# Kernel tuning notes

Hardware: AMD Instinct MI355X
Metric: run time of the kernel (lower is better)

## Reference

```python
import jax, jax.numpy as jnp
import numpy as np

B, R, L = 1024, 10, 512  # batch, num_rounds, lstm_size
EPS = 1e-10


def _gated(x, Wy, by, Wg, bg):
    # GatedTrans: tanh(Linear(x)) * sigmoid(Linear(x)); dropout is identity in eval
    return jnp.tanh(x @ Wy + by) * jax.nn.sigmoid(x @ Wg + bg)


def setup_inputs() -> dict:
    key = jax.random.key(0)
    ks = jax.random.split(key, 16)
    s_in = 1.0 / np.sqrt(2 * L)
    s_hid = 1.0 / np.sqrt(L)
    inp = {
        "hist": jax.random.normal(ks[0], (B, R, 2 * L), jnp.float32),
        "ques": jax.random.normal(ks[1], (B, R, 2 * L), jnp.float32),
        "noise": jax.random.uniform(ks[2], (B, R, R), jnp.float32),
        # H_embed GatedTrans params
        "Wy_h": jax.random.normal(ks[3], (2 * L, L), jnp.float32) * s_in,
        "by_h": jnp.zeros((L,), jnp.float32),
        "Wg_h": jax.random.normal(ks[4], (2 * L, L), jnp.float32) * s_in,
        "bg_h": jnp.zeros((L,), jnp.float32),
        # Q_embed GatedTrans params
        "Wy_q": jax.random.normal(ks[5], (2 * L, L), jnp.float32) * s_in,
        "by_q": jnp.zeros((L,), jnp.float32),
        "Wg_q": jax.random.normal(ks[6], (2 * L, L), jnp.float32) * s_in,
        "bg_q": jnp.zeros((L,), jnp.float32),
        # MLP: Linear(2L->L), Linear(L->1)
        "W1": jax.random.normal(ks[7], (2 * L, L), jnp.float32) * s_in,
        "b1": jnp.zeros((L,), jnp.float32),
        "W2": jax.random.normal(ks[8], (L, 1), jnp.float32) * s_hid,
        "b2": jnp.zeros((1,), jnp.float32),
        # att: Linear(2->1)
        "Wa": jax.random.normal(ks[9], (2, 1), jnp.float32) * 0.7,
        "ba": jnp.zeros((1,), jnp.float32),
    }
    return inp


def _forward(hist, ques, noise, Wy_h, by_h, Wg_h, bg_h, Wy_q, by_q, Wg_q, bg_q,
             W1, b1, W2, b2, Wa, ba):
    h = _gated(hist, Wy_h, by_h, Wg_h, bg_h)  # [B,R,L], indexed by j (history round)
    q = _gated(ques, Wy_q, by_q, Wg_q, bg_q)  # [B,R,L], indexed by i (question round)
    # MLP layer 1 on concat(h_j, q_i) without materializing the 2L concat:
    sh = h @ W1[:L] + b1            # [B,R,L] (j part + bias)
    sq = q @ W1[L:]                 # [B,R,L] (i part)
    hid = sq[:, :, None, :] + sh[:, None, :, :]  # [B,R(i),R(j),L]
    score = (hid @ W2 + b2)[..., 0]              # [B,R,R]
    # delta_t = cumsum over rows of lower-triangular ones
    tri = jnp.tril(jnp.ones((R, R), jnp.float32))
    delta_t = jnp.cumsum(tri, axis=0)            # [R,R]
    # att Linear(2->1) on concat(score, delta_t)
    logits = score * Wa[0, 0] + delta_t * Wa[1, 0] + ba[0]  # [B,R,R]
    # per-round Gumbel softmax over prefix [:i+1], vectorized with tril mask
    g = -jnp.log(EPS - jnp.log(noise + EPS))     # Gumbel(0,1) noise
    mask = tri.astype(bool)                       # [R,R], True for j<=i
    z = jnp.where(mask, logits + g, -1e9)
    y_soft = jax.nn.softmax(z, axis=-1)           # temperature = 1
    one_hot = jax.nn.one_hot(jnp.argmax(z, axis=-1), R, dtype=logits.dtype)
    # straight-through: value = one_hot, gradient flows through y_soft (valid cols only)
    y = one_hot + (y_soft - jax.lax.stop_gradient(y_soft)) * tri
    return y


def reference(hist, ques, noise, Wy_h, by_h, Wg_h, bg_h, Wy_q, by_q, Wg_q, bg_q,
              W1, b1, W2, b2, Wa, ba):
    return _forward(hist, ques, noise, Wy_h, by_h, Wg_h, bg_h, Wy_q, by_q,
                    Wg_q, bg_q, W1, b1, W2, b2, Wa, ba)
```

## Files before the change

### kernel.cpp

```cpp
#include <hip/hip_runtime.h>
#include <math.h>

typedef float f4 __attribute__((ext_vector_type(4)));
typedef float f32x4 __attribute__((ext_vector_type(4)));
typedef _Float16 h4 __attribute__((ext_vector_type(4)));
typedef _Float16 h8 __attribute__((ext_vector_type(8)));

#define NB 1024
#define NR 10
#define NL 512
#define NM (NB*NR)
#define NK (2*NL)

#define BIMG_OFF   131072ull
#define BIMG_EMBED 4194304ull
#define AIMG_OFF   (BIMG_OFF + 2ull*BIMG_EMBED)
#define AIMG_EMBED (80ull*32ull*16384ull)
#define WS_NEED2   (AIMG_OFF + 2ull*AIMG_EMBED)

#define SCALE_A 16.0f
#define SCALE_B 512.0f
#define INV_SCALE (1.0f/8192.0f)

__device__ __forceinline__ void gl_lds16(const void* g, void* s) {
    __builtin_amdgcn_global_load_lds(
        (const __attribute__((address_space(1))) unsigned int*)g,
        (__attribute__((address_space(3))) unsigned int*)s, 16, 0, 0);
}

__global__ __launch_bounds__(256) void k_prep(
    const float* __restrict__ hist, const float* __restrict__ ques,
    const float* __restrict__ Wy_h, const float* __restrict__ Wg_h,
    const float* __restrict__ Wy_q, const float* __restrict__ Wg_q,
    const float* __restrict__ W1, const float* __restrict__ b1,
    const float* __restrict__ W2, const float* __restrict__ b2,
    char* __restrict__ Aimg, char* __restrict__ Bimg,
    float* __restrict__ vh, float* __restrict__ vq, float* __restrict__ cc,
    float* __restrict__ tzero)
{
    __shared__ float Ws[32][68];
    __shared__ float red[4];
    const int bid = blockIdx.x;
    const int t = threadIdx.x;

    if (bid < 5120) {
        const int rb = bid % 80, ks = (bid / 80) % 32, z = bid / 2560;
        const float* X = z ? ques : hist;
        char* dst = Aimg + (size_t)z*AIMG_EMBED + ((size_t)(rb*32 + ks))*16384;
        #pragma unroll
        for (int i = 0; i < 2; ++i) {
            const int m   = i*4 + (t >> 6);
            const int row = m*16 + (t & 15);
            const int kg  = (t >> 4) & 3;
            const float* src = X + (size_t)(rb*128 + row)*NK + ks*32 + kg*8;
            f4 a0 = *(const f4*)src;
            f4 a1 = *(const f4*)(src + 4);
            h8 hi, lo;
            #pragma unroll
            for (int j = 0; j < 4; ++j) {
                float x0 = a0[j] * SCALE_A;
                _Float16 h0 = (_Float16)x0;
                hi[j] = h0; lo[j] = (_Float16)(x0 - (float)h0);
                float x1 = a1[j] * SCALE_A;
                _Float16 h1 = (_Float16)x1;
                hi[4+j] = h1; lo[4+j] = (_Float16)(x1 - (float)h1);
            }
            *(h8*)(dst + i*4096 + t*16) = hi;
            *(h8*)(dst + 8192 + i*4096 + t*16) = lo;
        }
    } else if (bid < 6144) {
        const int wb = bid - 5120;
        const int nh = wb % 8, ks = (wb / 8) % 32, mi = wb / 256;
        const float* W = (mi==0) ? Wy_h : (mi==1) ? Wg_h : (mi==2) ? Wy_q : Wg_q;
        const int emb = mi >> 1, nfb = (mi & 1) * 4;
        const int kl = t >> 4, nl4 = (t & 15) * 4;
        #pragma unroll
        for (int i = 0; i < 2; ++i) {
            f4 wv = *(const f4*)(W + (size_t)(ks*32 + kl + 16*i)*NL + nh*64 + nl4);
            *(f4*)&Ws[kl + 16*i][nl4] = wv;
        }
        __syncthreads();
        const int kg = t >> 6, nl = t & 63;
        h8 hi, lo;
        #pragma unroll
        for (int e8 = 0; e8 < 8; ++e8) {
            float x = Ws[kg*8 + e8][nl] * SCALE_B;
            _Float16 h = (_Float16)x;
            hi[e8] = h;
            lo[e8] = (_Float16)(x - (float)h);
        }
        const int nf  = nfb + (nl >> 4);
        const int l16 = (nl & 15) + 16*kg;
        char* p = Bimg + (size_t)emb*BIMG_EMBED
                + ((size_t)(nh*32 + ks)*2)*8192 + nf*1024 + l16*16;
        *(h8*)p = hi;
        *(h8*)(p + 8192) = lo;
    } else if (bid < 7169) {
        const int o = bid - 6144;
        const float* row = (o < 1024) ? (W1 + (size_t)o*NL) : b1;
        float s = fmaf(row[t], W2[t], row[t+256]*W2[t+256]);
        #pragma unroll
        for (int d = 1; d < 64; d <<= 1) s += __shfl_xor(s, d);
        if ((t & 63) == 0) red[t >> 6] = s;
        __syncthreads();
        if (t == 0) {
            float tot = red[0] + red[1] + red[2] + red[3];
            if (o < 512) vh[o] = tot;
            else if (o < 1024) vq[o-512] = tot;
            else cc[0] = tot + b2[0];
        }
    } else {
        const int zb = bid - 7169;
        f4 zz = {0.f, 0.f, 0.f, 0.f};
        *(f4*)(tzero + (size_t)zb*1024 + t*4) = zz;
    }
}

__global__ __launch_bounds__(256, 2) void k_embed_mfma3(
    const char* __restrict__ Aimg, const char* __restrict__ Bimg,
    const float* __restrict__ by_h, const float* __restrict__ bg_h,
    const float* __restrict__ by_q, const float* __restrict__ bg_q,
    const float* __restrict__ vv, float* __restrict__ tout)
{
    const int z = blockIdx.z, nt = blockIdx.y, rb = blockIdx.x;
    const float* by = z ? by_q : by_h;
    const float* bg = z ? bg_q : bg_h;
    const float* v  = vv + z*NL;
    float* tptr = tout + (size_t)z*NM;
    const char* At = Aimg + (size_t)z*AIMG_EMBED + ((size_t)rb*32)*16384;
    const char* Bt = Bimg + (size_t)z*BIMG_EMBED + (size_t)nt*32*16384;

    __shared__ char smem[65536];

    const int t = threadIdx.x;
    const int l = t & 63, w = t >> 6;
    const int wr = w >> 1, wc = w & 1;

    f32x4 acc[4][4];
    #pragma unroll
    for (int m = 0; m < 4; ++m)
      #pragma unroll
      for (int n = 0; n < 4; ++n) { f32x4 zz = {0.f,0.f,0.f,0.f}; acc[m][n] = zz; }

    auto stage = [&](int b, int ksrc) {
        const char* ga = At + (size_t)ksrc*16384 + w*4096 + l*16;
        const char* gb = Bt + (size_t)ksrc*16384 + w*4096 + l*16;
        char* da = smem + b*32768 + w*4096;
        char* db = smem + b*32768 + 16384 + w*4096;
        #pragma unroll
        for (int j = 0; j < 4; ++j) {
            gl_lds16(ga + j*1024, da + j*1024);
            gl_lds16(gb + j*1024, db + j*1024);
        }
    };

    stage(0, 0);
    stage(1, 1);
    asm volatile("s_waitcnt vmcnt(8)" ::: "memory");
    __builtin_amdgcn_s_barrier();

    #pragma unroll 2
    for (int ks = 0; ks < 32; ++ks) {
        const int cur = ks & 1;
        const char* sA = smem + cur*32768;
        const char* sB = sA + 16384;

        h8 av[4][2], bv[4][2];
        #pragma unroll
        for (int m = 0; m < 4; ++m)
          #pragma unroll
          for (int s = 0; s < 2; ++s)
            av[m][s] = *(const h8*)(sA + s*8192 + (wr*4 + m)*1024 + l*16);
        #pragma unroll
        for (int fn = 0; fn < 4; ++fn) {
            const int nf = (fn < 2) ? (wc*2 + fn) : (4 + wc*2 + (fn - 2));
            #pragma unroll
            for (int s = 0; s < 2; ++s)
                bv[fn][s] = *(const h8*)(sB + s*8192 + nf*1024 + l*16);
        }
        asm volatile("s_waitcnt lgkmcnt(0)" ::: "memory");
        __builtin_amdgcn_sched_barrier(0);
        __builtin_amdgcn_s_barrier();
        if (ks + 2 < 32) stage(cur, ks + 2);

        __builtin_amdgcn_s_setprio(1);
        #pragma unroll
        for (int m = 0; m < 4; ++m)
          #pragma unroll
          for (int fn = 0; fn < 4; ++fn) {
            acc[m][fn] = __builtin_amdgcn_mfma_f32_16x16x32_f16(av[m][0], bv[fn][0], acc[m][fn], 0, 0, 0);
            acc[m][fn] = __builtin_amdgcn_mfma_f32_16x16x32_f16(av[m][0], bv[fn][1], acc[m][fn], 0, 0, 0);
            acc[m][fn] = __builtin_amdgcn_mfma_f32_16x16x32_f16(av[m][1], bv[fn][0], acc[m][fn], 0, 0, 0);
          }
        __builtin_amdgcn_s_setprio(0);

        if (ks < 30)       asm volatile("s_waitcnt vmcnt(8)" ::: "memory");
        else if (ks == 30) asm volatile("s_waitcnt vmcnt(0)" ::: "memory");
        if (ks < 31) __builtin_amdgcn_s_barrier();
    }

    const int coll = l & 15, rg = l >> 4;
    #pragma unroll
    for (int m = 0; m < 4; ++m) {
      #pragma unroll
      for (int r = 0; r < 4; ++r) {
        float ps = 0.0f;
        #pragma unroll
        for (int n = 0; n < 2; ++n) {
            const int c = nt*64 + wc*32 + n*16 + coll;
            float y = acc[m][n  ][r]*INV_SCALE + by[c];
            float g = acc[m][n+2][r]*INV_SCALE + bg[c];
            ps += v[c] * (tanhf(y) * (1.0f/(1.0f + expf(-g))));
        }
        ps += __shfl_xor(ps, 1);
        ps += __shfl_xor(ps, 2);
        ps += __shfl_xor(ps, 4);
        ps += __shfl_xor(ps, 8);
        if (coll == 0)
            atomicAdd(&tptr[rb*128 + wr*64 + m*16 + rg*4 + r], ps);
      }
    }
}

__global__ __launch_bounds__(256) void k_vcalc2(const float* __restrict__ W1,
    const float* __restrict__ b1, const float* __restrict__ W2,
    const float* __restrict__ b2, float* __restrict__ vh,
    float* __restrict__ vq, float* __restrict__ cc)
{
    const int o = blockIdx.x;
    const float* row = (o < 1024) ? (W1 + (size_t)o*NL) : b1;
    const int t = threadIdx.x;
    float s = fmaf(row[t], W2[t], row[t+256]*W2[t+256]);
    #pragma unroll
    for (int d = 1; d < 64; d <<= 1) s += __shfl_xor(s, d);
    __shared__ float red[4];
    if ((t & 63) == 0) red[t >> 6] = s;
    __syncthreads();
    if (t == 0) {
        float tot = red[0] + red[1] + red[2] + red[3];
        if (o < 512) vh[o] = tot;
        else if (o < 1024) vq[o-512] = tot;
        else cc[0] = tot + b2[0];
    }
}

__global__ __launch_bounds__(256) void k_embed(const float* __restrict__ X,
    const float* __restrict__ Wy, const float* __restrict__ by,
    const float* __restrict__ Wg, const float* __restrict__ bg,
    const float* __restrict__ v, float* __restrict__ tout)
{
    __shared__ float As[32][68];
    __shared__ float Bys[32][64];
    __shared__ float Bgs[32][64];
    const int tid  = threadIdx.x;
    const int row0 = blockIdx.x * 64;
    const int c0   = blockIdx.y * 64;
    const int tx = tid & 15, ty = tid >> 4;
    float accy[4][4] = {};
    float accg[4][4] = {};
    const int arow = tid >> 3;
    const int ak   = (tid & 7) << 2;
    const int bk   = tid >> 4;
    const int bc   = (tid & 15) << 2;
    const float* Xp0 = X + (size_t)(row0 + arow)*NK + ak;
    const float* Xp1 = Xp0 + (size_t)32*NK;
    for (int k0 = 0; k0 < NK; k0 += 32) {
        f4 a0 = *(const f4*)(Xp0 + k0);
        f4 a1 = *(const f4*)(Xp1 + k0);
        f4 y0 = *(const f4*)&Wy[(size_t)(k0+bk   )*NL + c0 + bc];
        f4 y1 = *(const f4*)&Wy[(size_t)(k0+bk+16)*NL + c0 + bc];
        f4 g0 = *(const f4*)&Wg[(size_t)(k0+bk   )*NL + c0 + bc];
        f4 g1 = *(const f4*)&Wg[(size_t)(k0+bk+16)*NL + c0 + bc];
        #pragma unroll
        for (int j = 0; j < 4; ++j) {
            As[ak+j][arow]      = a0[j];
            As[ak+j][arow + 32] = a1[j];
        }
        *(f4*)&Bys[bk   ][bc] = y0;
        *(f4*)&Bys[bk+16][bc] = y1;
        *(f4*)&Bgs[bk   ][bc] = g0;
        *(f4*)&Bgs[bk+16][bc] = g1;
        __syncthreads();
        #pragma unroll
        for (int kk = 0; kk < 32; ++kk) {
            f4 a   = *(const f4*)&As [kk][ty<<2];
            f4 byv = *(const f4*)&Bys[kk][tx<<2];
            f4 bgv = *(const f4*)&Bgs[kk][tx<<2];
            #pragma unroll
            for (int rr = 0; rr < 4; ++rr)
                #pragma unroll
                for (int cc2 = 0; cc2 < 4; ++cc2) {
                    accy[rr][cc2] = fmaf(a[rr], byv[cc2], accy[rr][cc2]);
                    accg[rr][cc2] = fmaf(a[rr], bgv[cc2], accg[rr][cc2]);
                }
        }
        __syncthreads();
    }
    float rowsum[4] = {0.f, 0.f, 0.f, 0.f};
    #pragma unroll
    for (int rr = 0; rr < 4; ++rr)
        #pragma unroll
        for (int cc2 = 0; cc2 < 4; ++cc2) {
            int c = c0 + (tx<<2) + cc2;
            float xy = accy[rr][cc2] + by[c];
            float xg = accg[rr][cc2] + bg[c];
            float hv = tanhf(xy) * (1.0f / (1.0f + expf(-xg)));
            rowsum[rr] += v[c] * hv;
        }
    float* red = &As[0][0];
    #pragma unroll
    for (int rr = 0; rr < 4; ++rr) red[(ty*4 + rr)*16 + tx] = rowsum[rr];
    __syncthreads();
    if (tid < 64) {
        float s = 0.0f;
        #pragma unroll
        for (int t2 = 0; t2 < 16; ++t2) s += red[tid*16 + t2];
        atomicAdd(&tout[row0 + tid], s);
    }
}

__global__ __launch_bounds__(256) void k_final(const float* __restrict__ th,
    const float* __restrict__ tq, const float* __restrict__ cc,
    const float* __restrict__ noise, const float* __restrict__ Wa,
    const float* __restrict__ ba, float* __restrict__ out)
{
    int idx = blockIdx.x*256 + threadIdx.x;
    if (idx >= NM) return;
    int b = idx / NR, i = idx % NR;
    float wa0 = Wa[0], wa1 = Wa[1], bav = ba[0], c = cc[0];
    float ti = tq[idx];
    const float EPS = 1e-10f;
    float best = -3.0e38f; int am = 0;
    for (int j = 0; j < NR; ++j) {
        float zz;
        if (j <= i) {
            float n = noise[idx*NR + j];
            float g = -logf(EPS - logf(n + EPS));
            float score = ti + th[b*NR + j] + c;
            zz = score*wa0 + (float)(i - j + 1)*wa1 + bav + g;
        } else {
            zz = -1.0e9f;
        }
        if (zz > best) { best = zz; am = j; }
    }
    #pragma unroll
    for (int j = 0; j < NR; ++j) out[idx*NR + j] = (j == am) ? 1.0f : 0.0f;
}

extern "C" void kernel_launch(void* const* d_in, const int* in_sizes, int n_in,
                              void* d_out, int out_size, void* d_ws, size_t ws_size,
                              hipStream_t stream) {
    (void)in_sizes; (void)n_in; (void)out_size;
    const float* hist  = (const float*)d_in[0];
    const float* ques  = (const float*)d_in[1];
    const float* noise = (const float*)d_in[2];
    const float* Wy_h  = (const float*)d_in[3];
    const float* by_h  = (const float*)d_in[4];
    const float* Wg_h  = (const float*)d_in[5];
    const float* bg_h  = (const float*)d_in[6];
    const float* Wy_q  = (const float*)d_in[7];
    const float* by_q  = (const float*)d_in[8];
    const float* Wg_q  = (const float*)d_in[9];
    const float* bg_q  = (const float*)d_in[10];
    const float* W1    = (const float*)d_in[11];
    const float* b1    = (const float*)d_in[12];
    const float* W2    = (const float*)d_in[13];
    const float* b2    = (const float*)d_in[14];
    const float* Wa    = (const float*)d_in[15];
    const float* ba    = (const float*)d_in[16];
    float* out = (float*)d_out;

    float* ws     = (float*)d_ws;
    float* t_h    = ws;
    float* t_q    = ws + NM;
    float* v_h    = ws + 2*NM;
    float* v_q    = v_h + NL;
    float* cconst = v_q + NL;

    if (ws_size >= WS_NEED2) {
        char* Bimg = (char*)d_ws + BIMG_OFF;
        char* Aimg = (char*)d_ws + AIMG_OFF;
        k_prep<<<7189, 256, 0, stream>>>(hist, ques, Wy_h, Wg_h, Wy_q, Wg_q,
            W1, b1, W2, b2, Aimg, Bimg, v_h, v_q, cconst, t_h);
        k_embed_mfma3<<<dim3(80, 8, 2), 256, 0, stream>>>(Aimg, Bimg,
            by_h, bg_h, by_q, bg_q, v_h, t_h);
    } else {
        hipMemsetAsync(t_h, 0, 2*NM*sizeof(float), stream);
        k_vcalc2<<<1025, 256, 0, stream>>>(W1, b1, W2, b2, v_h, v_q, cconst);
        dim3 g(NM/64, NL/64);
        k_embed<<<g, 256, 0, stream>>>(hist, Wy_h, by_h, Wg_h, bg_h, v_h, t_h);
        k_embed<<<g, 256, 0, stream>>>(ques, Wy_q, by_q, Wg_q, bg_q, v_q, t_q);
    }
    k_final<<<(NM + 255)/256, 256, 0, stream>>>(t_h, t_q, cconst, noise, Wa, ba, out);
}
```

Before: 277.7 us.

## Fuse activation fp16 hi/lo split into the MFMA GEMM mainloop

The separate prep pass that converted hist/ques to split-fp16 images in workspace is removed. The GEMM kernel now loads fp32 activations into registers two steps ahead, splits them into hi/lo halves, and writes them into the next LDS buffer itself, while B is still staged with direct global-to-LDS loads. This drops a full write and reread of the activation image (about 80 MB) and shrinks the prep kernel. In exchange the mainloop carries extra VALU conversion work and register pressure, and each activation tile is read and converted again by all 8 N-tile blocks.

```diff
diff --git a/kernel.cpp b/kernel.cpp
--- a/kernel.cpp
+++ b/kernel.cpp
@@ -14,9 +14,7 @@
 
 #define BIMG_OFF   131072ull
 #define BIMG_EMBED 4194304ull
-#define AIMG_OFF   (BIMG_OFF + 2ull*BIMG_EMBED)
-#define AIMG_EMBED (80ull*32ull*16384ull)
-#define WS_NEED2   (AIMG_OFF + 2ull*AIMG_EMBED)
+#define WS_NEED    (BIMG_OFF + 2ull*BIMG_EMBED)
 
 #define SCALE_A 16.0f
 #define SCALE_B 512.0f
@@ -29,12 +27,11 @@
 }
 
 __global__ __launch_bounds__(256) void k_prep(
-    const float* __restrict__ hist, const float* __restrict__ ques,
     const float* __restrict__ Wy_h, const float* __restrict__ Wg_h,
     const float* __restrict__ Wy_q, const float* __restrict__ Wg_q,
     const float* __restrict__ W1, const float* __restrict__ b1,
     const float* __restrict__ W2, const float* __restrict__ b2,
-    char* __restrict__ Aimg, char* __restrict__ Bimg,
+    char* __restrict__ Bimg,
     float* __restrict__ vh, float* __restrict__ vq, float* __restrict__ cc,
     float* __restrict__ tzero)
 {
@@ -43,34 +40,8 @@
     const int bid = blockIdx.x;
     const int t = threadIdx.x;
 
-    if (bid < 5120) {
-        const int rb = bid % 80, ks = (bid / 80) % 32, z = bid / 2560;
-        const float* X = z ? ques : hist;
-        char* dst = Aimg + (size_t)z*AIMG_EMBED + ((size_t)(rb*32 + ks))*16384;
-        #pragma unroll
-        for (int i = 0; i < 2; ++i) {
-            const int m   = i*4 + (t >> 6);
-            const int row = m*16 + (t & 15);
-            const int kg  = (t >> 4) & 3;
-            const float* src = X + (size_t)(rb*128 + row)*NK + ks*32 + kg*8;
-            f4 a0 = *(const f4*)src;
-            f4 a1 = *(const f4*)(src + 4);
-            h8 hi, lo;
-            #pragma unroll
-            for (int j = 0; j < 4; ++j) {
-                float x0 = a0[j] * SCALE_A;
-                _Float16 h0 = (_Float16)x0;
-                hi[j] = h0; lo[j] = (_Float16)(x0 - (float)h0);
-                float x1 = a1[j] * SCALE_A;
-                _Float16 h1 = (_Float16)x1;
-                hi[4+j] = h1; lo[4+j] = (_Float16)(x1 - (float)h1);
-            }
-            *(h8*)(dst + i*4096 + t*16) = hi;
-            *(h8*)(dst + 8192 + i*4096 + t*16) = lo;
-        }
-    } else if (bid < 6144) {
-        const int wb = bid - 5120;
-        const int nh = wb % 8, ks = (wb / 8) % 32, mi = wb / 256;
+    if (bid < 1024) {
+        const int nh = bid % 8, ks = (bid / 8) % 32, mi = bid / 256;
         const float* W = (mi==0) ? Wy_h : (mi==1) ? Wg_h : (mi==2) ? Wy_q : Wg_q;
         const int emb = mi >> 1, nfb = (mi & 1) * 4;
         const int kl = t >> 4, nl4 = (t & 15) * 4;
@@ -95,8 +66,8 @@
                 + ((size_t)(nh*32 + ks)*2)*8192 + nf*1024 + l16*16;
         *(h8*)p = hi;
         *(h8*)(p + 8192) = lo;
-    } else if (bid < 7169) {
-        const int o = bid - 6144;
+    } else if (bid < 2049) {
+        const int o = bid - 1024;
         const float* row = (o < 1024) ? (W1 + (size_t)o*NL) : b1;
         float s = fmaf(row[t], W2[t], row[t+256]*W2[t+256]);
         #pragma unroll
@@ -110,24 +81,25 @@
             else cc[0] = tot + b2[0];
         }
     } else {
-        const int zb = bid - 7169;
+        const int zb = bid - 2049;
         f4 zz = {0.f, 0.f, 0.f, 0.f};
         *(f4*)(tzero + (size_t)zb*1024 + t*4) = zz;
     }
 }
 
-__global__ __launch_bounds__(256, 2) void k_embed_mfma3(
-    const char* __restrict__ Aimg, const char* __restrict__ Bimg,
+__global__ __launch_bounds__(256, 2) void k_embed_mfma4(
+    const float* __restrict__ hist, const float* __restrict__ ques,
+    const char* __restrict__ Bimg,
     const float* __restrict__ by_h, const float* __restrict__ bg_h,
     const float* __restrict__ by_q, const float* __restrict__ bg_q,
     const float* __restrict__ vv, float* __restrict__ tout)
 {
     const int z = blockIdx.z, nt = blockIdx.y, rb = blockIdx.x;
+    const float* X  = z ? ques : hist;
     const float* by = z ? by_q : by_h;
     const float* bg = z ? bg_q : bg_h;
     const float* v  = vv + z*NL;
     float* tptr = tout + (size_t)z*NM;
-    const char* At = Aimg + (size_t)z*AIMG_EMBED + ((size_t)rb*32)*16384;
     const char* Bt = Bimg + (size_t)z*BIMG_EMBED + (size_t)nt*32*16384;
 
     __shared__ char smem[65536];
@@ -136,34 +108,64 @@
     const int l = t & 63, w = t >> 6;
     const int wr = w >> 1, wc = w & 1;
 
+    const int am0 = t >> 6;
+    const float* src1 = X + (size_t)(rb*128 + am0*16 + (t & 15))*NK + ((t >> 4) & 3)*8;
+    const float* src2 = src1 + (size_t)64*NK;
+    const int aw1 = am0*1024 + (t & 63)*16;
+    const int aw2 = aw1 + 4096;
+
+    f4 ar0, ar1, ar2, ar3;
+    auto loadA = [&](int ksrc) {
+        const float* p1 = src1 + ksrc*32;
+        const float* p2 = src2 + ksrc*32;
+        ar0 = *(const f4*)p1; ar1 = *(const f4*)(p1 + 4);
+        ar2 = *(const f4*)p2; ar3 = *(const f4*)(p2 + 4);
+    };
+    auto splitA = [&](char* base) {
+        h8 hi1, lo1, hi2, lo2;
+        #pragma unroll
+        for (int j = 0; j < 4; ++j) {
+            float x0 = ar0[j]*SCALE_A; _Float16 h0 = (_Float16)x0;
+            hi1[j] = h0;   lo1[j] = (_Float16)(x0 - (float)h0);
+            float x1 = ar1[j]*SCALE_A; _Float16 h1 = (_Float16)x1;
+            hi1[4+j] = h1; lo1[4+j] = (_Float16)(x1 - (float)h1);
+            float x2 = ar2[j]*SCALE_A; _Float16 h2 = (_Float16)x2;
+            hi2[j] = h2;   lo2[j] = (_Float16)(x2 - (float)h2);
+            float x3 = ar3[j]*SCALE_A; _Float16 h3 = (_Float16)x3;
+            hi2[4+j] = h3; lo2[4+j] = (_Float16)(x3 - (float)h3);
+        }
+        *(h8*)(base + aw1) = hi1;  *(h8*)(base + 8192 + aw1) = lo1;
+        *(h8*)(base + aw2) = hi2;  *(h8*)(base + 8192 + aw2) = lo2;
+    };
+    auto stageB = [&](int buf, int ksrc) {
+        const char* gb = Bt + (size_t)ksrc*16384 + w*4096 + l*16;
+        char* db = smem + buf*32768 + 16384 + w*4096;
+        #pragma unroll
+        for (int j = 0; j < 4; ++j) gl_lds16(gb + j*1024, db + j*1024);
+    };
+
     f32x4 acc[4][4];
     #pragma unroll
     for (int m = 0; m < 4; ++m)
       #pragma unroll
       for (int n = 0; n < 4; ++n) { f32x4 zz = {0.f,0.f,0.f,0.f}; acc[m][n] = zz; }
 
-    auto stage = [&](int b, int ksrc) {
-        const char* ga = At + (size_t)ksrc*16384 + w*4096 + l*16;
-        const char* gb = Bt + (size_t)ksrc*16384 + w*4096 + l*16;
-        char* da = smem + b*32768 + w*4096;
-        char* db = smem + b*32768 + 16384 + w*4096;
-        #pragma unroll
-        for (int j = 0; j < 4; ++j) {
-            gl_lds16(ga + j*1024, da + j*1024);
-            gl_lds16(gb + j*1024, db + j*1024);
-        }
-    };
-
-    stage(0, 0);
-    stage(1, 1);
-    asm volatile("s_waitcnt vmcnt(8)" ::: "memory");
+    loadA(0);
+    splitA(smem);
+    loadA(1);
+    stageB(0, 0);
+    stageB(1, 1);
+    asm volatile("s_waitcnt lgkmcnt(0)" ::: "memory");
+    asm volatile("s_waitcnt vmcnt(4)" ::: "memory");
     __builtin_amdgcn_s_barrier();
 
     #pragma unroll 2
     for (int ks = 0; ks < 32; ++ks) {
-        const int cur = ks & 1;
+        const int cur = ks & 1, nxt = cur ^ 1;
         const char* sA = smem + cur*32768;
         const char* sB = sA + 16384;
+
+        if (ks < 31) splitA(smem + nxt*32768);
 
         h8 av[4][2], bv[4][2];
         #pragma unroll
@@ -178,10 +180,14 @@
             for (int s = 0; s < 2; ++s)
                 bv[fn][s] = *(const h8*)(sB + s*8192 + nf*1024 + l*16);
         }
+
+        if (ks < 30) loadA(ks + 2);
+
         asm volatile("s_waitcnt lgkmcnt(0)" ::: "memory");
         __builtin_amdgcn_sched_barrier(0);
         __builtin_amdgcn_s_barrier();
-        if (ks + 2 < 32) stage(cur, ks + 2);
+
+        if (ks < 30) stageB(cur, ks + 2);
 
         __builtin_amdgcn_s_setprio(1);
         #pragma unroll
@@ -377,12 +383,11 @@
     float* v_q    = v_h + NL;
     float* cconst = v_q + NL;
 
-    if (ws_size >= WS_NEED2) {
+    if (ws_size >= WS_NEED) {
         char* Bimg = (char*)d_ws + BIMG_OFF;
-        char* Aimg = (char*)d_ws + AIMG_OFF;
-        k_prep<<<7189, 256, 0, stream>>>(hist, ques, Wy_h, Wg_h, Wy_q, Wg_q,
-            W1, b1, W2, b2, Aimg, Bimg, v_h, v_q, cconst, t_h);
-        k_embed_mfma3<<<dim3(80, 8, 2), 256, 0, stream>>>(Aimg, Bimg,
+        k_prep<<<2069, 256, 0, stream>>>(Wy_h, Wg_h, Wy_q, Wg_q,
+            W1, b1, W2, b2, Bimg, v_h, v_q, cconst, t_h);
+        k_embed_mfma4<<<dim3(80, 8, 2), 256, 0, stream>>>(hist, ques, Bimg,
             by_h, bg_h, by_q, bg_q, v_h, t_h);
     } else {
         hipMemsetAsync(t_h, 0, 2*NM*sizeof(float), stream);
```

New measurement: 306.8 us. 1.1x slower.

## Halve embed GEMM N-tile and use triple-buffered LDS pipeline

Applied to the files above, without the earlier changes.

The embed MFMA kernel now computes 32 output columns per block instead of 64, doubling the grid to 80x16x2, and each block loads only its half of the B tile. LDS staging moves from double to triple buffering, so the next-next stage is issued before the current LDS reads and one barrier per iteration is removed. The aim is more blocks for load balance across CUs and better overlap of global loads with MFMA work. In exchange, A tiles are re-read twice as often and each block does less MFMA work per load, and twice as many atomics hit the output.

```diff
diff --git a/kernel.cpp b/kernel.cpp
--- a/kernel.cpp
+++ b/kernel.cpp
@@ -3,7 +3,6 @@
 
 typedef float f4 __attribute__((ext_vector_type(4)));
 typedef float f32x4 __attribute__((ext_vector_type(4)));
-typedef _Float16 h4 __attribute__((ext_vector_type(4)));
 typedef _Float16 h8 __attribute__((ext_vector_type(8)));
 
 #define NB 1024
@@ -116,102 +115,105 @@
     }
 }
 
-__global__ __launch_bounds__(256, 2) void k_embed_mfma3(
+__global__ __launch_bounds__(256, 2) void k_embed_mfma5(
     const char* __restrict__ Aimg, const char* __restrict__ Bimg,
     const float* __restrict__ by_h, const float* __restrict__ bg_h,
     const float* __restrict__ by_q, const float* __restrict__ bg_q,
     const float* __restrict__ vv, float* __restrict__ tout)
 {
-    const int z = blockIdx.z, nt = blockIdx.y, rb = blockIdx.x;
+    const int z = blockIdx.z, ntn = blockIdx.y, rb = blockIdx.x;
     const float* by = z ? by_q : by_h;
     const float* bg = z ? bg_q : bg_h;
     const float* v  = vv + z*NL;
     float* tptr = tout + (size_t)z*NM;
     const char* At = Aimg + (size_t)z*AIMG_EMBED + ((size_t)rb*32)*16384;
-    const char* Bt = Bimg + (size_t)z*BIMG_EMBED + (size_t)nt*32*16384;
-
-    __shared__ char smem[65536];
+    const int nt_old = ntn >> 1, half = ntn & 1;
+    const char* Bt = Bimg + (size_t)z*BIMG_EMBED + (size_t)nt_old*32*16384;
+
+    __shared__ char smem[73728];
 
     const int t = threadIdx.x;
     const int l = t & 63, w = t >> 6;
     const int wr = w >> 1, wc = w & 1;
 
-    f32x4 acc[4][4];
+    const int c0i = 2*w, c1i = 2*w + 1;
+    const int s0 = c0i >> 2, nfl0 = c0i & 3;
+    const int s1 = c1i >> 2, nfl1 = c1i & 3;
+    const int nfo0 = (nfl0 < 2) ? (half*2 + nfl0) : (4 + half*2 + (nfl0 - 2));
+    const int nfo1 = (nfl1 < 2) ? (half*2 + nfl1) : (4 + half*2 + (nfl1 - 2));
+
+    auto stage = [&](int buf, int ks) {
+        char* base = smem + buf*24576;
+        const char* ga = At + (size_t)ks*16384 + w*4096 + l*16;
+        #pragma unroll
+        for (int j = 0; j < 4; ++j)
+            gl_lds16(ga + j*1024, base + w*4096 + j*1024);
+        const char* gb = Bt + (size_t)ks*16384;
+        gl_lds16(gb + s0*8192 + nfo0*1024 + l*16,
+                 base + 16384 + s0*4096 + nfl0*1024 + l*16);
+        gl_lds16(gb + s1*8192 + nfo1*1024 + l*16,
+                 base + 16384 + s1*4096 + nfl1*1024 + l*16);
+    };
+
+    f32x4 acc[4][2];
     #pragma unroll
     for (int m = 0; m < 4; ++m)
       #pragma unroll
-      for (int n = 0; n < 4; ++n) { f32x4 zz = {0.f,0.f,0.f,0.f}; acc[m][n] = zz; }
-
-    auto stage = [&](int b, int ksrc) {
-        const char* ga = At + (size_t)ksrc*16384 + w*4096 + l*16;
-        const char* gb = Bt + (size_t)ksrc*16384 + w*4096 + l*16;
-        char* da = smem + b*32768 + w*4096;
-        char* db = smem + b*32768 + 16384 + w*4096;
-        #pragma unroll
-        for (int j = 0; j < 4; ++j) {
-            gl_lds16(ga + j*1024, da + j*1024);
-            gl_lds16(gb + j*1024, db + j*1024);
-        }
-    };
+      for (int n = 0; n < 2; ++n) { f32x4 zz = {0.f,0.f,0.f,0.f}; acc[m][n] = zz; }
 
     stage(0, 0);
     stage(1, 1);
-    asm volatile("s_waitcnt vmcnt(8)" ::: "memory");
+    asm volatile("s_waitcnt vmcnt(6)" ::: "memory");
     __builtin_amdgcn_s_barrier();
 
-    #pragma unroll 2
+    int cur = 0, nx2 = 2;
     for (int ks = 0; ks < 32; ++ks) {
-        const int cur = ks & 1;
-        const char* sA = smem + cur*32768;
+        const char* sA = smem + cur*24576;
         const char* sB = sA + 16384;
 
-        h8 av[4][2], bv[4][2];
+        if (ks + 2 < 32) stage(nx2, ks + 2);
+
+        h8 av[4][2], bv[2][2];
         #pragma unroll
         for (int m = 0; m < 4; ++m)
           #pragma unroll
           for (int s = 0; s < 2; ++s)
             av[m][s] = *(const h8*)(sA + s*8192 + (wr*4 + m)*1024 + l*16);
         #pragma unroll
-        for (int fn = 0; fn < 4; ++fn) {
-            const int nf = (fn < 2) ? (wc*2 + fn) : (4 + wc*2 + (fn - 2));
-            #pragma unroll
-            for (int s = 0; s < 2; ++s)
-                bv[fn][s] = *(const h8*)(sB + s*8192 + nf*1024 + l*16);
-        }
-        asm volatile("s_waitcnt lgkmcnt(0)" ::: "memory");
-        __builtin_amdgcn_sched_barrier(0);
-        __builtin_amdgcn_s_barrier();
-        if (ks + 2 < 32) stage(cur, ks + 2);
+        for (int fn = 0; fn < 2; ++fn)
+          #pragma unroll
+          for (int s = 0; s < 2; ++s)
+            bv[fn][s] = *(const h8*)(sB + s*4096 + (fn*2 + wc)*1024 + l*16);
 
         __builtin_amdgcn_s_setprio(1);
         #pragma unroll
         for (int m = 0; m < 4; ++m)
           #pragma unroll
-          for (int fn = 0; fn < 4; ++fn) {
+          for (int fn = 0; fn < 2; ++fn) {
             acc[m][fn] = __builtin_amdgcn_mfma_f32_16x16x32_f16(av[m][0], bv[fn][0], acc[m][fn], 0, 0, 0);
             acc[m][fn] = __builtin_amdgcn_mfma_f32_16x16x32_f16(av[m][0], bv[fn][1], acc[m][fn], 0, 0, 0);
             acc[m][fn] = __builtin_amdgcn_mfma_f32_16x16x32_f16(av[m][1], bv[fn][0], acc[m][fn], 0, 0, 0);
           }
         __builtin_amdgcn_s_setprio(0);
 
-        if (ks < 30)       asm volatile("s_waitcnt vmcnt(8)" ::: "memory");
+        if (ks < 30)       asm volatile("s_waitcnt vmcnt(6)" ::: "memory");
         else if (ks == 30) asm volatile("s_waitcnt vmcnt(0)" ::: "memory");
         if (ks < 31) __builtin_amdgcn_s_barrier();
+
+        cur = (cur == 2) ? 0 : cur + 1;
+        nx2 = (nx2 == 2) ? 0 : nx2 + 1;
     }
 
     const int coll = l & 15, rg = l >> 4;
+    const int c = ntn*32 + wc*16 + coll;
+    const float byc = by[c], bgc = bg[c], vc = v[c];
     #pragma unroll
     for (int m = 0; m < 4; ++m) {
       #pragma unroll
       for (int r = 0; r < 4; ++r) {
-        float ps = 0.0f;
-        #pragma unroll
-        for (int n = 0; n < 2; ++n) {
-            const int c = nt*64 + wc*32 + n*16 + coll;
-            float y = acc[m][n  ][r]*INV_SCALE + by[c];
-            float g = acc[m][n+2][r]*INV_SCALE + bg[c];
-            ps += v[c] * (tanhf(y) * (1.0f/(1.0f + expf(-g))));
-        }
+        float y = acc[m][0][r]*INV_SCALE + byc;
+        float g = acc[m][1][r]*INV_SCALE + bgc;
+        float ps = vc * (tanhf(y) * (1.0f/(1.0f + expf(-g))));
         ps += __shfl_xor(ps, 1);
         ps += __shfl_xor(ps, 2);
         ps += __shfl_xor(ps, 4);
@@ -382,7 +384,7 @@
         char* Aimg = (char*)d_ws + AIMG_OFF;
         k_prep<<<7189, 256, 0, stream>>>(hist, ques, Wy_h, Wg_h, Wy_q, Wg_q,
             W1, b1, W2, b2, Aimg, Bimg, v_h, v_q, cconst, t_h);
-        k_embed_mfma3<<<dim3(80, 8, 2), 256, 0, stream>>>(Aimg, Bimg,
+        k_embed_mfma5<<<dim3(80, 16, 2), 256, 0, stream>>>(Aimg, Bimg,
             by_h, bg_h, by_q, bg_q, v_h, t_h);
     } else {
         hipMemsetAsync(t_h, 0, 2*NM*sizeof(float), stream);
```

Measured after the change: 310.3 us. 11.7% more time.

## Enlarge GEMM M-tile from 128 to 160 rows to cut grid to 1024 blocks

Applied to the files above, without the earlier changes.

Each workgroup now computes 160 rows (5 MFMA row fragments per wave instead of 4), so the embed grid shrinks from 80x8x2 to 64x8x2 = 1024 blocks. With 256 CUs at 2 blocks each, that is two full waves instead of a partial third wave. The A-image layout, prep kernel and LDS staging are all resized to match. The trade-off is more accumulator registers, 72KB of LDS per block (which may still allow 2 blocks per CU), and an extra vmcnt slot in the pipeline.

```diff
diff --git a/kernel.cpp b/kernel.cpp
--- a/kernel.cpp
+++ b/kernel.cpp
@@ -3,7 +3,6 @@
 
 typedef float f4 __attribute__((ext_vector_type(4)));
 typedef float f32x4 __attribute__((ext_vector_type(4)));
-typedef _Float16 h4 __attribute__((ext_vector_type(4)));
 typedef _Float16 h8 __attribute__((ext_vector_type(8)));
 
 #define NB 1024
@@ -15,7 +14,8 @@
 #define BIMG_OFF   131072ull
 #define BIMG_EMBED 4194304ull
 #define AIMG_OFF   (BIMG_OFF + 2ull*BIMG_EMBED)
-#define AIMG_EMBED (80ull*32ull*16384ull)
+#define ATILE      20480ull
+#define AIMG_EMBED (64ull*32ull*ATILE)
 #define WS_NEED2   (AIMG_OFF + 2ull*AIMG_EMBED)
 
 #define SCALE_A 16.0f
@@ -43,33 +43,36 @@
     const int bid = blockIdx.x;
     const int t = threadIdx.x;
 
-    if (bid < 5120) {
-        const int rb = bid % 80, ks = (bid / 80) % 32, z = bid / 2560;
+    if (bid < 4096) {
+        const int rb = bid % 64, ks = (bid / 64) % 32, z = bid / 2048;
         const float* X = z ? ques : hist;
-        char* dst = Aimg + (size_t)z*AIMG_EMBED + ((size_t)(rb*32 + ks))*16384;
-        #pragma unroll
-        for (int i = 0; i < 2; ++i) {
-            const int m   = i*4 + (t >> 6);
-            const int row = m*16 + (t & 15);
-            const int kg  = (t >> 4) & 3;
-            const float* src = X + (size_t)(rb*128 + row)*NK + ks*32 + kg*8;
-            f4 a0 = *(const f4*)src;
-            f4 a1 = *(const f4*)(src + 4);
-            h8 hi, lo;
-            #pragma unroll
-            for (int j = 0; j < 4; ++j) {
-                float x0 = a0[j] * SCALE_A;
-                _Float16 h0 = (_Float16)x0;
-                hi[j] = h0; lo[j] = (_Float16)(x0 - (float)h0);
-                float x1 = a1[j] * SCALE_A;
-                _Float16 h1 = (_Float16)x1;
-                hi[4+j] = h1; lo[4+j] = (_Float16)(x1 - (float)h1);
+        char* dst = Aimg + (size_t)z*AIMG_EMBED + ((size_t)(rb*32 + ks))*ATILE;
+        #pragma unroll
+        for (int i = 0; i < 3; ++i) {
+            const int unit = i*256 + t;
+            if (unit < 640) {
+                const int mf = unit >> 6, l = unit & 63;
+                const int row = mf*16 + (l & 15);
+                const int kg  = l >> 4;
+                const float* src = X + (size_t)(rb*160 + row)*NK + ks*32 + kg*8;
+                f4 a0 = *(const f4*)src;
+                f4 a1 = *(const f4*)(src + 4);
+                h8 hi, lo;
+                #pragma unroll
+                for (int j = 0; j < 4; ++j) {
+                    float x0 = a0[j] * SCALE_A;
+                    _Float16 h0 = (_Float16)x0;
+                    hi[j] = h0; lo[j] = (_Float16)(x0 - (float)h0);
+                    float x1 = a1[j] * SCALE_A;
+                    _Float16 h1 = (_Float16)x1;
+                    hi[4+j] = h1; lo[4+j] = (_Float16)(x1 - (float)h1);
+                }
+                *(h8*)(dst + mf*1024 + l*16) = hi;
+                *(h8*)(dst + 10240 + mf*1024 + l*16) = lo;
             }
-            *(h8*)(dst + i*4096 + t*16) = hi;
-            *(h8*)(dst + 8192 + i*4096 + t*16) = lo;
-        }
-    } else if (bid < 6144) {
-        const int wb = bid - 5120;
+        }
+    } else if (bid < 5120) {
+        const int wb = bid - 4096;
         const int nh = wb % 8, ks = (wb / 8) % 32, mi = wb / 256;
         const float* W = (mi==0) ? Wy_h : (mi==1) ? Wg_h : (mi==2) ? Wy_q : Wg_q;
         const int emb = mi >> 1, nfb = (mi & 1) * 4;
@@ -95,8 +98,8 @@
                 + ((size_t)(nh*32 + ks)*2)*8192 + nf*1024 + l16*16;
         *(h8*)p = hi;
         *(h8*)(p + 8192) = lo;
-    } else if (bid < 7169) {
-        const int o = bid - 6144;
+    } else if (bid < 6145) {
+        const int o = bid - 5120;
         const float* row = (o < 1024) ? (W1 + (size_t)o*NL) : b1;
         float s = fmaf(row[t], W2[t], row[t+256]*W2[t+256]);
         #pragma unroll
@@ -110,13 +113,13 @@
             else cc[0] = tot + b2[0];
         }
     } else {
-        const int zb = bid - 7169;
+        const int zb = bid - 6145;
         f4 zz = {0.f, 0.f, 0.f, 0.f};
         *(f4*)(tzero + (size_t)zb*1024 + t*4) = zz;
     }
 }
 
-__global__ __launch_bounds__(256, 2) void k_embed_mfma3(
+__global__ __launch_bounds__(256, 2) void k_embed_mfma6(
     const char* __restrict__ Aimg, const char* __restrict__ Bimg,
     const float* __restrict__ by_h, const float* __restrict__ bg_h,
     const float* __restrict__ by_q, const float* __restrict__ bg_q,
@@ -127,50 +130,51 @@
     const float* bg = z ? bg_q : bg_h;
     const float* v  = vv + z*NL;
     float* tptr = tout + (size_t)z*NM;
-    const char* At = Aimg + (size_t)z*AIMG_EMBED + ((size_t)rb*32)*16384;
+    const char* At = Aimg + (size_t)z*AIMG_EMBED + ((size_t)rb*32)*ATILE;
     const char* Bt = Bimg + (size_t)z*BIMG_EMBED + (size_t)nt*32*16384;
 
-    __shared__ char smem[65536];
+    __shared__ char smem[73728];
 
     const int t = threadIdx.x;
     const int l = t & 63, w = t >> 6;
     const int wr = w >> 1, wc = w & 1;
 
-    f32x4 acc[4][4];
-    #pragma unroll
-    for (int m = 0; m < 4; ++m)
+    f32x4 acc[5][4];
+    #pragma unroll
+    for (int m = 0; m < 5; ++m)
       #pragma unroll
       for (int n = 0; n < 4; ++n) { f32x4 zz = {0.f,0.f,0.f,0.f}; acc[m][n] = zz; }
 
     auto stage = [&](int b, int ksrc) {
-        const char* ga = At + (size_t)ksrc*16384 + w*4096 + l*16;
+        const char* ga = At + (size_t)ksrc*ATILE + w*5120 + l*16;
         const char* gb = Bt + (size_t)ksrc*16384 + w*4096 + l*16;
-        char* da = smem + b*32768 + w*4096;
-        char* db = smem + b*32768 + 16384 + w*4096;
-        #pragma unroll
-        for (int j = 0; j < 4; ++j) {
+        char* da = smem + b*36864 + w*5120;
+        char* db = smem + b*36864 + 20480 + w*4096;
+        #pragma unroll
+        for (int j = 0; j < 5; ++j)
             gl_lds16(ga + j*1024, da + j*1024);
+        #pragma unroll
+        for (int j = 0; j < 4; ++j)
             gl_lds16(gb + j*1024, db + j*1024);
-        }
     };
 
     stage(0, 0);
     stage(1, 1);
-    asm volatile("s_waitcnt vmcnt(8)" ::: "memory");
+    asm volatile("s_waitcnt vmcnt(9)" ::: "memory");
     __builtin_amdgcn_s_barrier();
 
     #pragma unroll 2
     for (int ks = 0; ks < 32; ++ks) {
         const int cur = ks & 1;
-        const char* sA = smem + cur*32768;
-        const char* sB = sA + 16384;
-
-        h8 av[4][2], bv[4][2];
-        #pragma unroll
-        for (int m = 0; m < 4; ++m)
+        const char* sA = smem + cur*36864;
+        const char* sB = sA + 20480;
+
+        h8 av[5][2], bv[4][2];
+        #pragma unroll
+        for (int m = 0; m < 5; ++m)
           #pragma unroll
           for (int s = 0; s < 2; ++s)
-            av[m][s] = *(const h8*)(sA + s*8192 + (wr*4 + m)*1024 + l*16);
+            av[m][s] = *(const h8*)(sA + s*10240 + (wr*5 + m)*1024 + l*16);
         #pragma unroll
         for (int fn = 0; fn < 4; ++fn) {
             const int nf = (fn < 2) ? (wc*2 + fn) : (4 + wc*2 + (fn - 2));
@@ -185,7 +189,7 @@
 
         __builtin_amdgcn_s_setprio(1);
         #pragma unroll
-        for (int m = 0; m < 4; ++m)
+        for (int m = 0; m < 5; ++m)
           #pragma unroll
           for (int fn = 0; fn < 4; ++fn) {
             acc[m][fn] = __builtin_amdgcn_mfma_f32_16x16x32_f16(av[m][0], bv[fn][0], acc[m][fn], 0, 0, 0);
@@ -194,14 +198,14 @@
           }
         __builtin_amdgcn_s_setprio(0);
 
-        if (ks < 30)       asm volatile("s_waitcnt vmcnt(8)" ::: "memory");
+        if (ks < 30)       asm volatile("s_waitcnt vmcnt(9)" ::: "memory");
         else if (ks == 30) asm volatile("s_waitcnt vmcnt(0)" ::: "memory");
         if (ks < 31) __builtin_amdgcn_s_barrier();
     }
 
     const int coll = l & 15, rg = l >> 4;
     #pragma unroll
-    for (int m = 0; m < 4; ++m) {
+    for (int m = 0; m < 5; ++m) {
       #pragma unroll
       for (int r = 0; r < 4; ++r) {
         float ps = 0.0f;
@@ -217,7 +221,7 @@
         ps += __shfl_xor(ps, 4);
         ps += __shfl_xor(ps, 8);
         if (coll == 0)
-            atomicAdd(&tptr[rb*128 + wr*64 + m*16 + rg*4 + r], ps);
+            atomicAdd(&tptr[rb*160 + wr*80 + m*16 + rg*4 + r], ps);
       }
     }
 }
@@ -380,9 +384,9 @@
     if (ws_size >= WS_NEED2) {
         char* Bimg = (char*)d_ws + BIMG_OFF;
         char* Aimg = (char*)d_ws + AIMG_OFF;
-        k_prep<<<7189, 256, 0, stream>>>(hist, ques, Wy_h, Wg_h, Wy_q, Wg_q,
+        k_prep<<<6165, 256, 0, stream>>>(hist, ques, Wy_h, Wg_h, Wy_q, Wg_q,
             W1, b1, W2, b2, Aimg, Bimg, v_h, v_q, cconst, t_h);
-        k_embed_mfma3<<<dim3(80, 8, 2), 256, 0, stream>>>(Aimg, Bimg,
+        k_embed_mfma6<<<dim3(64, 8, 2), 256, 0, stream>>>(Aimg, Bimg,
             by_h, bg_h, by_q, bg_q, v_h, t_h);
     } else {
         hipMemsetAsync(t_h, 0, 2*NM*sizeof(float), stream);
```

New measurement: 280.6 us. About the same (+1.0%).
